# Kernel optimization log

Hardware: AMD Instinct MI355X
Metric: run time of the kernel (lower is better)

Reference implementation:

```python
import jax, jax.numpy as jnp
import numpy as np

N_NODES = 50000
N_EDGES = 800000


def _sage_layer(h, src, dst, ew, Ws, Wn, b, activate):
    # DGL SAGEConv, aggregator_type='mean', with edge weights:
    # message m_e = ew_e * h_src ; neigh = mean over incoming edges (divide by in-degree)
    msg = h[src] * ew[:, None]                       # [E, F] irregular gather
    agg = jax.ops.segment_sum(msg, dst, num_segments=N_NODES)
    deg = jax.ops.segment_sum(jnp.ones_like(ew), dst, num_segments=N_NODES)
    h_neigh = agg / jnp.maximum(deg, 1.0)[:, None]   # zero for isolated nodes
    out = h @ Ws + h_neigh @ Wn + b                  # fc_self + fc_neigh + bias
    return jnp.tanh(out) if activate else out


def setup_inputs() -> dict:
    key = jax.random.key(0)
    ks = jax.random.split(key, 12)
    d = 64
    inp = {
        "b_z": jax.random.normal(ks[0], (N_NODES, d), dtype=jnp.float32),
        "edge_src": jax.random.randint(ks[1], (N_EDGES,), 0, N_NODES, dtype=jnp.int32),
        "edge_dst": jax.random.randint(ks[2], (N_EDGES,), 0, N_NODES, dtype=jnp.int32),
        "edge_weight": jax.random.uniform(ks[3], (N_EDGES,), dtype=jnp.float32),
        "Ws0": jax.random.normal(ks[4], (64, 32), dtype=jnp.float32) / np.sqrt(64),
        "Wn0": jax.random.normal(ks[5], (64, 32), dtype=jnp.float32) / np.sqrt(64),
        "b0": jnp.zeros((32,), jnp.float32),
        "Ws1": jax.random.normal(ks[6], (32, 16), dtype=jnp.float32) / np.sqrt(32),
        "Wn1": jax.random.normal(ks[7], (32, 16), dtype=jnp.float32) / np.sqrt(32),
        "b1": jnp.zeros((16,), jnp.float32),
        "Ws2": jax.random.normal(ks[8], (16, 1), dtype=jnp.float32) / np.sqrt(16),
        "Wn2": jax.random.normal(ks[9], (16, 1), dtype=jnp.float32) / np.sqrt(16),
        "b2": jnp.zeros((1,), jnp.float32),
        "b_size": 500,
    }
    return inp


def reference(b_z, edge_src, edge_dst, edge_weight,
              Ws0, Wn0, b0, Ws1, Wn1, b1, Ws2, Wn2, b2, b_size):
    h = _sage_layer(b_z, edge_src, edge_dst, edge_weight, Ws0, Wn0, b0, True)
    h = _sage_layer(h, edge_src, edge_dst, edge_weight, Ws1, Wn1, b1, True)
    h = _sage_layer(h, edge_src, edge_dst, edge_weight, Ws2, Wn2, b2, False)
    x_hat = h.reshape(b_size, -1)
    return x_hat
```

## Files before the change

### kernel.cpp

```cpp
#include <hip/hip_runtime.h>
#include <hip/hip_bf16.h>

#define N_NODES 50000
#define N_EDGES 800000
#define BLK 256
#define NRANGE 256
#define RNG 196
#define NPART 256
#define EPB 3125
#define PCAP 44
#define SCAP 48

#define EW_SCALE (1.0f / 65535.0f)

__device__ inline void unpack8(uint4 g, float* f) {
    f[0] = __uint_as_float(g.x << 16); f[1] = __uint_as_float(g.x & 0xffff0000u);
    f[2] = __uint_as_float(g.y << 16); f[3] = __uint_as_float(g.y & 0xffff0000u);
    f[4] = __uint_as_float(g.z << 16); f[5] = __uint_as_float(g.z & 0xffff0000u);
    f[6] = __uint_as_float(g.w << 16); f[7] = __uint_as_float(g.w & 0xffff0000u);
}
__device__ inline void unpack4(uint2 g, float* f) {
    f[0] = __uint_as_float(g.x << 16); f[1] = __uint_as_float(g.x & 0xffff0000u);
    f[2] = __uint_as_float(g.y << 16); f[3] = __uint_as_float(g.y & 0xffff0000u);
}

__global__ void pack_premul0_kernel(const int* __restrict__ src,
                                    const float* __restrict__ ew,
                                    unsigned int* __restrict__ pay,
                                    const float* __restrict__ b_z,
                                    const float* __restrict__ Wn0,
                                    const float* __restrict__ Ws0,
                                    const float* __restrict__ b0,
                                    __hip_bfloat16* __restrict__ hW0,
                                    float* __restrict__ hSelf0, int N, int E) {
    int tid = threadIdx.x;
    for (int e = blockIdx.x * BLK + tid; e < E; e += gridDim.x * BLK) {
        unsigned int q = __float2uint_rn(ew[e] * 65535.0f);
        pay[e] = (q << 16) | (unsigned int)src[e];
    }

    __shared__ float sWn[64 * 32];
    __shared__ float sWs[64 * 32];
    __shared__ float sb[32];
    __shared__ float sh[8 * 65];
    for (int i = tid; i < 64 * 32; i += BLK) { sWn[i] = Wn0[i]; sWs[i] = Ws0[i]; }
    if (tid < 32) sb[tid] = b0[tid];
    const int nch = (N + 7) / 8;
    int r = tid >> 5, j = tid & 31;
    for (int c = blockIdx.x; c < nch; c += gridDim.x) {
        __syncthreads();
        int nodeBase = c * 8;
        for (int i = tid; i < 8 * 64; i += BLK) {
            int rr = i >> 6, k = i & 63;
            int n = nodeBase + rr;
            sh[rr * 65 + k] = (n < N) ? b_z[(size_t)n * 64 + k] : 0.f;
        }
        __syncthreads();
        int n = nodeBase + r;
        if (n < N) {
            float an = 0.f, as = 0.f;
#pragma unroll
            for (int k = 0; k < 64; ++k) {
                float hk = sh[r * 65 + k];
                an += hk * sWn[k * 32 + j];
                as += hk * sWs[k * 32 + j];
            }
            hW0[(size_t)n * 32 + j] = __float2bfloat16(an);
            hSelf0[(size_t)n * 32 + j] = as + sb[j];
        }
    }
}

__global__ void partA_kernel(const int* __restrict__ dst,
                             const unsigned int* __restrict__ pay,
                             uint2* __restrict__ lists,
                             int* __restrict__ pcnt) {
    __shared__ uint2 sSorted[EPB];
    __shared__ int hist[NRANGE];
    __shared__ int pfx[NRANGE];
    __shared__ int cur[NRANGE];
    int tid = threadIdx.x;
    int b = blockIdx.x;
    int base = b * EPB;

    hist[tid] = 0;
    __syncthreads();
    for (int i = tid; i < EPB; i += BLK)
        atomicAdd(&hist[dst[base + i] / RNG], 1);
    __syncthreads();
    {
        int v = hist[tid];
        pfx[tid] = v;
        __syncthreads();
        for (int off = 1; off < NRANGE; off <<= 1) {
            int t = (tid >= off) ? pfx[tid - off] : 0;
            __syncthreads();
            pfx[tid] += t;
            __syncthreads();
        }
        int incl = pfx[tid];
        __syncthreads();
        pfx[tid] = incl - v;
        cur[tid] = incl - v;
        __syncthreads();
    }
    for (int i = tid; i < EPB; i += BLK) {
        int e = base + i;
        int d = dst[e];
        int pos = atomicAdd(&cur[d / RNG], 1);
        sSorted[pos] = make_uint2(pay[e], (unsigned int)d);
    }
    __syncthreads();
    for (int i = tid; i < EPB; i += BLK) {
        int lo = 0, hi = NRANGE - 1;
        while (lo < hi) { int mid = (lo + hi + 1) >> 1; if (pfx[mid] <= i) lo = mid; else hi = mid - 1; }
        int idx = i - pfx[lo];
        if (idx < PCAP)
            lists[((size_t)lo * NPART + b) * PCAP + idx] = sSorted[i];
    }
    pcnt[tid * NPART + b] = min(hist[tid], PCAP);
}

__global__ void partB_kernel(const uint2* __restrict__ lists,
                             const int* __restrict__ pcnt,
                             unsigned int* __restrict__ bucket,
                             int* __restrict__ counts, int N) {
    __shared__ unsigned int lslot[RNG * SCAP];
    __shared__ int lcnt[RNG];
    __shared__ int scnt[NPART];
    __shared__ int spfx[NPART];
    int tid = threadIdx.x;
    int r = blockIdx.x;
    int node0 = r * RNG;
    int nn = min(RNG, N - node0);
    if (nn <= 0) return;

    for (int i = tid; i < RNG; i += BLK) lcnt[i] = 0;
    scnt[tid] = pcnt[r * NPART + tid];
    __syncthreads();
    {
        int v = scnt[tid];
        spfx[tid] = v;
        __syncthreads();
        for (int off = 1; off < NPART; off <<= 1) {
            int t = (tid >= off) ? spfx[tid - off] : 0;
            __syncthreads();
            spfx[tid] += t;
            __syncthreads();
        }
        int incl = spfx[tid];
        __syncthreads();
        spfx[tid] = incl - v;
        __syncthreads();
    }
    int T = spfx[NPART - 1] + scnt[NPART - 1];
    for (int j = tid; j < T; j += BLK) {
        int lo = 0, hi = NPART - 1;
        while (lo < hi) { int mid = (lo + hi + 1) >> 1; if (spfx[mid] <= j) lo = mid; else hi = mid - 1; }
        int idx = j - spfx[lo];
        uint2 en = lists[((size_t)r * NPART + lo) * PCAP + idx];
        int node = (int)en.y - node0;
        int pos = atomicAdd(&lcnt[node], 1);
        if (pos < SCAP) lslot[node * SCAP + pos] = en.x;
    }
    __syncthreads();
    unsigned int* __restrict__ gb = bucket + (size_t)node0 * SCAP;
    int tot = nn * SCAP;
    for (int i = tid; i < tot; i += BLK) gb[i] = lslot[i];
    for (int i = tid; i < nn; i += BLK) counts[node0 + i] = min(lcnt[i], SCAP);
}

__global__ void agg0_kernel(const __hip_bfloat16* __restrict__ hW0,
                            const float* __restrict__ hSelf0,
                            const int* __restrict__ cnts,
                            const unsigned int* __restrict__ bucket,
                            const float* __restrict__ Wn1,
                            const float* __restrict__ Ws1,
                            const float* __restrict__ b1,
                            __hip_bfloat16* __restrict__ hW1,
                            float* __restrict__ hSelf1, int N) {
    __shared__ float sWn[32 * 16];
    __shared__ float sWs[32 * 16];
    __shared__ float sb[16];
    __shared__ float sh2[64 * 33];
    int tid = threadIdx.x;
    for (int i = tid; i < 32 * 16; i += BLK) { sWn[i] = Wn1[i]; sWs[i] = Ws1[i]; }
    if (tid < 16) sb[tid] = b1[tid];

    const uint4* __restrict__ tab = (const uint4*)hW0;
    int nodeBase = blockIdx.x * 64;
    int r = tid >> 2;
    int l = tid & 3;
    int n = nodeBase + r;
    if (n < N) {
        int cnt = cnts[n];
        int cn  = min(cnt, SCAP);
        const unsigned int* __restrict__ ep = bucket + (size_t)n * SCAP;
        float acc[8];
#pragma unroll
        for (int t = 0; t < 8; ++t) acc[t] = 0.f;
        int k = 0;
        for (; k + 8 <= cn; k += 8) {
            uint4 ev0 = *(const uint4*)(ep + k);
            uint4 ev1 = *(const uint4*)(ep + k + 4);
            unsigned int ee[8] = { ev0.x, ev0.y, ev0.z, ev0.w,
                                   ev1.x, ev1.y, ev1.z, ev1.w };
            uint4 g[8];
            float w[8];
#pragma unroll
            for (int u = 0; u < 8; ++u) {
                g[u] = tab[(size_t)(ee[u] & 0xffffu) * 4 + l];
                w[u] = (float)(ee[u] >> 16) * EW_SCALE;
            }
#pragma unroll
            for (int u = 0; u < 8; ++u) {
                float f[8];
                unpack8(g[u], f);
#pragma unroll
                for (int t = 0; t < 8; ++t) acc[t] += w[u] * f[t];
            }
        }
        for (; k < cn; ++k) {
            unsigned int e = ep[k];
            float w = (float)(e >> 16) * EW_SCALE;
            uint4 g = tab[(size_t)(e & 0xffffu) * 4 + l];
            float f[8];
            unpack8(g, f);
#pragma unroll
            for (int t = 0; t < 8; ++t) acc[t] += w * f[t];
        }
        float invdeg = 1.0f / fmaxf((float)cnt, 1.0f);
        const float4* __restrict__ hs = (const float4*)(hSelf0 + (size_t)n * 32);
        float4 s0 = hs[l * 2], s1 = hs[l * 2 + 1];
        float sf[8] = { s0.x, s0.y, s0.z, s0.w, s1.x, s1.y, s1.z, s1.w };
#pragma unroll
        for (int t = 0; t < 8; ++t)
            sh2[r * 33 + l * 8 + t] = tanhf(acc[t] * invdeg + sf[t]);
    }
    __syncthreads();
    for (int idx = tid; idx < 64 * 16; idx += BLK) {
        int r2 = idx >> 4, j2 = idx & 15;
        int n2 = nodeBase + r2;
        if (n2 < N) {
            float an = 0.f, as = 0.f;
#pragma unroll
            for (int k = 0; k < 32; ++k) {
                float hk = sh2[r2 * 33 + k];
                an += hk * sWn[k * 16 + j2];
                as += hk * sWs[k * 16 + j2];
            }
            hW1[(size_t)n2 * 16 + j2] = __float2bfloat16(an);
            hSelf1[(size_t)n2 * 16 + j2] = as + sb[j2];
        }
    }
}

__global__ void agg1_kernel(const __hip_bfloat16* __restrict__ hW1,
                            const float* __restrict__ hSelf1,
                            const int* __restrict__ cnts,
                            const unsigned int* __restrict__ bucket,
                            const float* __restrict__ Wn2,
                            const float* __restrict__ Ws2,
                            const float* __restrict__ b2,
                            float* __restrict__ hWf,
                            float* __restrict__ hSelf2, int N) {
    int tid = threadIdx.x;
    int r = tid >> 2;
    int l = tid & 3;
    int n = blockIdx.x * 64 + r;
    if (n >= N) return;

    const uint2* __restrict__ tab = (const uint2*)hW1;
    int cnt = cnts[n];
    int cn  = min(cnt, SCAP);
    const unsigned int* __restrict__ ep = bucket + (size_t)n * SCAP;
    float acc[4];
#pragma unroll
    for (int t = 0; t < 4; ++t) acc[t] = 0.f;
    int k = 0;
    for (; k + 8 <= cn; k += 8) {
        uint4 ev0 = *(const uint4*)(ep + k);
        uint4 ev1 = *(const uint4*)(ep + k + 4);
        unsigned int ee[8] = { ev0.x, ev0.y, ev0.z, ev0.w,
                               ev1.x, ev1.y, ev1.z, ev1.w };
        uint2 g[8];
        float w[8];
#pragma unroll
        for (int u = 0; u < 8; ++u) {
            g[u] = tab[(size_t)(ee[u] & 0xffffu) * 4 + l];
            w[u] = (float)(ee[u] >> 16) * EW_SCALE;
        }
#pragma unroll
        for (int u = 0; u < 8; ++u) {
            float f[4];
            unpack4(g[u], f);
#pragma unroll
            for (int t = 0; t < 4; ++t) acc[t] += w[u] * f[t];
        }
    }
    for (; k < cn; ++k) {
        unsigned int e = ep[k];
        float w = (float)(e >> 16) * EW_SCALE;
        uint2 g = tab[(size_t)(e & 0xffffu) * 4 + l];
        float f[4];
        unpack4(g, f);
#pragma unroll
        for (int t = 0; t < 4; ++t) acc[t] += w * f[t];
    }
    float invdeg = 1.0f / fmaxf((float)cnt, 1.0f);
    const float4* __restrict__ hs = (const float4*)(hSelf1 + (size_t)n * 16);
    float4 sv = hs[l];
    float sf[4] = { sv.x, sv.y, sv.z, sv.w };
    float t2 = 0.f, t3 = 0.f;
#pragma unroll
    for (int t = 0; t < 4; ++t) {
        float hv = tanhf(acc[t] * invdeg + sf[t]);
        t2 += hv * Wn2[l * 4 + t];
        t3 += hv * Ws2[l * 4 + t];
    }
    t2 += __shfl_xor(t2, 1, 4); t2 += __shfl_xor(t2, 2, 4);
    t3 += __shfl_xor(t3, 1, 4); t3 += __shfl_xor(t3, 2, 4);
    if (l == 0) {
        hWf[n] = t2;
        hSelf2[n] = t3 + b2[0];
    }
}

__global__ void agg_final_kernel(const float* __restrict__ hWf,
                                 const float* __restrict__ hSelf2,
                                 const int* __restrict__ cnts,
                                 const unsigned int* __restrict__ bucket,
                                 float* __restrict__ out, int N) {
    int sub = threadIdx.x & 15;
    int r   = threadIdx.x >> 4;
    int n   = blockIdx.x * 16 + r;
    if (n >= N) return;
    int cnt = cnts[n];
    int cn  = min(cnt, SCAP);
    const unsigned int* __restrict__ ep = bucket + (size_t)n * SCAP;
    float a = 0.f;
    for (int k = sub; k < cn; k += 16) {
        unsigned int e = ep[k];
        a += ((float)(e >> 16) * EW_SCALE) * hWf[e & 0xffffu];
    }
#pragma unroll
    for (int m = 8; m >= 1; m >>= 1) a += __shfl_xor(a, m, 16);
    if (sub == 0) {
        float invdeg = 1.0f / fmaxf((float)cnt, 1.0f);
        out[n] = a * invdeg + hSelf2[n];
    }
}

extern "C" void kernel_launch(void* const* d_in, const int* in_sizes, int n_in,
                              void* d_out, int out_size, void* d_ws, size_t ws_size,
                              hipStream_t stream) {
    const float* b_z = (const float*)d_in[0];
    const int*   src = (const int*)d_in[1];
    const int*   dst = (const int*)d_in[2];
    const float* ew  = (const float*)d_in[3];
    const float* Ws0 = (const float*)d_in[4];
    const float* Wn0 = (const float*)d_in[5];
    const float* b0  = (const float*)d_in[6];
    const float* Ws1 = (const float*)d_in[7];
    const float* Wn1 = (const float*)d_in[8];
    const float* b1  = (const float*)d_in[9];
    const float* Ws2 = (const float*)d_in[10];
    const float* Wn2 = (const float*)d_in[11];
    const float* b2  = (const float*)d_in[12];

    const int N = N_NODES;
    const int E = N_EDGES;
    const int GRID_E = 2048;

    unsigned int* pay    = (unsigned int*)d_ws;
    uint2*        lists  = (uint2*)(pay + E);
    int*          pcnt   = (int*)(lists + (size_t)NRANGE * NPART * PCAP);
    int*          counts = pcnt + NRANGE * NPART;
    unsigned int* bucket = (unsigned int*)(counts + N);
    __hip_bfloat16* hW0  = (__hip_bfloat16*)(bucket + (size_t)N * SCAP);
    __hip_bfloat16* hW1  = hW0 + (size_t)N * 32;
    float* hWf    = (float*)(hW1 + (size_t)N * 16);
    float* hSelf0 = hWf + N;
    float* hSelf1 = hSelf0 + (size_t)N * 32;
    float* hSelf2 = hSelf1 + (size_t)N * 16;
    float* outp   = (float*)d_out;

    pack_premul0_kernel<<<GRID_E, BLK, 0, stream>>>(
        src, ew, pay, b_z, Wn0, Ws0, b0, hW0, hSelf0, N, E);
    partA_kernel<<<NPART, BLK, 0, stream>>>(dst, pay, lists, pcnt);
    partB_kernel<<<NRANGE, BLK, 0, stream>>>(lists, pcnt, bucket, counts, N);
    agg0_kernel<<<(N + 63) / 64, BLK, 0, stream>>>(
        hW0, hSelf0, counts, bucket, Wn1, Ws1, b1, hW1, hSelf1, N);
    agg1_kernel<<<(N + 63) / 64, BLK, 0, stream>>>(
        hW1, hSelf1, counts, bucket, Wn2, Ws2, b2, hWf, hSelf2, N);
    agg_final_kernel<<<(N + 15) / 16, BLK, 0, stream>>>(
        hWf, hSelf2, counts, bucket, outp, N);
}
```

Baseline: 105.9 us.

## Fuse layer-0 premultiply with edge partitioning into one block-specialized kernel

Merges the premultiply and payload-pack kernel with the partA edge-partition kernel. The first 256 blocks partition edges and build the packed payload inline from src/ew, while the remaining blocks do the layer-0 dense premultiply. This removes one launch and the global round trip of the intermediate payload array, and lets the two independent jobs overlap. In exchange, the unioned shared-memory buffer is sized for the larger partition branch, which may lower occupancy for the matmul blocks, and the premultiply now runs on fewer blocks.

```diff
diff --git a/kernel.cpp b/kernel.cpp
--- a/kernel.cpp
+++ b/kernel.cpp
@@ -10,6 +10,7 @@
 #define EPB 3125
 #define PCAP 44
 #define SCAP 48
+#define GRID_F 2048
 
 #define EW_SCALE (1.0f / 65535.0f)
 
@@ -24,101 +25,98 @@
     f[2] = __uint_as_float(g.y << 16); f[3] = __uint_as_float(g.y & 0xffff0000u);
 }
 
-__global__ void pack_premul0_kernel(const int* __restrict__ src,
-                                    const float* __restrict__ ew,
-                                    unsigned int* __restrict__ pay,
-                                    const float* __restrict__ b_z,
-                                    const float* __restrict__ Wn0,
-                                    const float* __restrict__ Ws0,
-                                    const float* __restrict__ b0,
-                                    __hip_bfloat16* __restrict__ hW0,
-                                    float* __restrict__ hSelf0, int N, int E) {
+__global__ void premul0_partA_kernel(const float* __restrict__ b_z,
+                                     const int* __restrict__ src,
+                                     const int* __restrict__ dst,
+                                     const float* __restrict__ ew,
+                                     const float* __restrict__ Wn0,
+                                     const float* __restrict__ Ws0,
+                                     const float* __restrict__ b0,
+                                     __hip_bfloat16* __restrict__ hW0,
+                                     float* __restrict__ hSelf0,
+                                     uint2* __restrict__ lists,
+                                     int* __restrict__ pcnt, int N) {
+    __shared__ __align__(16) unsigned char SMEM[28080];
     int tid = threadIdx.x;
-    for (int e = blockIdx.x * BLK + tid; e < E; e += gridDim.x * BLK) {
-        unsigned int q = __float2uint_rn(ew[e] * 65535.0f);
-        pay[e] = (q << 16) | (unsigned int)src[e];
-    }
-
-    __shared__ float sWn[64 * 32];
-    __shared__ float sWs[64 * 32];
-    __shared__ float sb[32];
-    __shared__ float sh[8 * 65];
-    for (int i = tid; i < 64 * 32; i += BLK) { sWn[i] = Wn0[i]; sWs[i] = Ws0[i]; }
-    if (tid < 32) sb[tid] = b0[tid];
-    const int nch = (N + 7) / 8;
-    int r = tid >> 5, j = tid & 31;
-    for (int c = blockIdx.x; c < nch; c += gridDim.x) {
-        __syncthreads();
-        int nodeBase = c * 8;
-        for (int i = tid; i < 8 * 64; i += BLK) {
-            int rr = i >> 6, k = i & 63;
-            int n = nodeBase + rr;
-            sh[rr * 65 + k] = (n < N) ? b_z[(size_t)n * 64 + k] : 0.f;
-        }
-        __syncthreads();
-        int n = nodeBase + r;
-        if (n < N) {
-            float an = 0.f, as = 0.f;
-#pragma unroll
-            for (int k = 0; k < 64; ++k) {
-                float hk = sh[r * 65 + k];
-                an += hk * sWn[k * 32 + j];
-                as += hk * sWs[k * 32 + j];
-            }
-            hW0[(size_t)n * 32 + j] = __float2bfloat16(an);
-            hSelf0[(size_t)n * 32 + j] = as + sb[j];
-        }
-    }
-}
-
-__global__ void partA_kernel(const int* __restrict__ dst,
-                             const unsigned int* __restrict__ pay,
-                             uint2* __restrict__ lists,
-                             int* __restrict__ pcnt) {
-    __shared__ uint2 sSorted[EPB];
-    __shared__ int hist[NRANGE];
-    __shared__ int pfx[NRANGE];
-    __shared__ int cur[NRANGE];
-    int tid = threadIdx.x;
-    int b = blockIdx.x;
-    int base = b * EPB;
-
-    hist[tid] = 0;
-    __syncthreads();
-    for (int i = tid; i < EPB; i += BLK)
-        atomicAdd(&hist[dst[base + i] / RNG], 1);
-    __syncthreads();
-    {
-        int v = hist[tid];
-        pfx[tid] = v;
-        __syncthreads();
-        for (int off = 1; off < NRANGE; off <<= 1) {
-            int t = (tid >= off) ? pfx[tid - off] : 0;
-            __syncthreads();
-            pfx[tid] += t;
-            __syncthreads();
-        }
-        int incl = pfx[tid];
-        __syncthreads();
-        pfx[tid] = incl - v;
-        cur[tid] = incl - v;
-        __syncthreads();
-    }
-    for (int i = tid; i < EPB; i += BLK) {
-        int e = base + i;
-        int d = dst[e];
-        int pos = atomicAdd(&cur[d / RNG], 1);
-        sSorted[pos] = make_uint2(pay[e], (unsigned int)d);
-    }
-    __syncthreads();
-    for (int i = tid; i < EPB; i += BLK) {
-        int lo = 0, hi = NRANGE - 1;
-        while (lo < hi) { int mid = (lo + hi + 1) >> 1; if (pfx[mid] <= i) lo = mid; else hi = mid - 1; }
-        int idx = i - pfx[lo];
-        if (idx < PCAP)
-            lists[((size_t)lo * NPART + b) * PCAP + idx] = sSorted[i];
-    }
-    pcnt[tid * NPART + b] = min(hist[tid], PCAP);
+    int bid = blockIdx.x;
+
+    if (bid < NPART) {
+        uint2* sSorted = (uint2*)SMEM;
+        int* hist = (int*)(SMEM + 25000);
+        int* pfx  = (int*)(SMEM + 26024);
+        int* cur  = (int*)(SMEM + 27048);
+        int base = bid * EPB;
+        hist[tid] = 0;
+        __syncthreads();
+        for (int i = tid; i < EPB; i += BLK)
+            atomicAdd(&hist[dst[base + i] / RNG], 1);
+        __syncthreads();
+        {
+            int v = hist[tid];
+            pfx[tid] = v;
+            __syncthreads();
+            for (int off = 1; off < NRANGE; off <<= 1) {
+                int t = (tid >= off) ? pfx[tid - off] : 0;
+                __syncthreads();
+                pfx[tid] += t;
+                __syncthreads();
+            }
+            int incl = pfx[tid];
+            __syncthreads();
+            pfx[tid] = incl - v;
+            cur[tid] = incl - v;
+            __syncthreads();
+        }
+        for (int i = tid; i < EPB; i += BLK) {
+            int e = base + i;
+            int d = dst[e];
+            unsigned int q = __float2uint_rn(ew[e] * 65535.0f);
+            unsigned int py = (q << 16) | (unsigned int)src[e];
+            int pos = atomicAdd(&cur[d / RNG], 1);
+            sSorted[pos] = make_uint2(py, (unsigned int)d);
+        }
+        __syncthreads();
+        for (int i = tid; i < EPB; i += BLK) {
+            int lo = 0, hi = NRANGE - 1;
+            while (lo < hi) { int mid = (lo + hi + 1) >> 1; if (pfx[mid] <= i) lo = mid; else hi = mid - 1; }
+            int idx = i - pfx[lo];
+            if (idx < PCAP)
+                lists[((size_t)lo * NPART + bid) * PCAP + idx] = sSorted[i];
+        }
+        pcnt[tid * NPART + bid] = min(hist[tid], PCAP);
+    } else {
+        float* sWn = (float*)SMEM;
+        float* sWs = (float*)(SMEM + 8192);
+        float* sb  = (float*)(SMEM + 16384);
+        float* sh  = (float*)(SMEM + 16512);
+        for (int i = tid; i < 64 * 32; i += BLK) { sWn[i] = Wn0[i]; sWs[i] = Ws0[i]; }
+        if (tid < 32) sb[tid] = b0[tid];
+        const int nch = (N + 7) / 8;
+        const int stride = GRID_F - NPART;
+        int r = tid >> 5, j = tid & 31;
+        for (int c = bid - NPART; c < nch; c += stride) {
+            __syncthreads();
+            int nodeBase = c * 8;
+            for (int i = tid; i < 8 * 64; i += BLK) {
+                int rr = i >> 6, k = i & 63;
+                int n = nodeBase + rr;
+                sh[rr * 65 + k] = (n < N) ? b_z[(size_t)n * 64 + k] : 0.f;
+            }
+            __syncthreads();
+            int n = nodeBase + r;
+            if (n < N) {
+                float an = 0.f, as = 0.f;
+#pragma unroll
+                for (int k = 0; k < 64; ++k) {
+                    float hk = sh[r * 65 + k];
+                    an += hk * sWn[k * 32 + j];
+                    as += hk * sWs[k * 32 + j];
+                }
+                hW0[(size_t)n * 32 + j] = __float2bfloat16(an);
+                hSelf0[(size_t)n * 32 + j] = as + sb[j];
+            }
+        }
+    }
 }
 
 __global__ void partB_kernel(const uint2* __restrict__ lists,
@@ -369,11 +367,8 @@
     const float* b2  = (const float*)d_in[12];
 
     const int N = N_NODES;
-    const int E = N_EDGES;
-    const int GRID_E = 2048;
-
-    unsigned int* pay    = (unsigned int*)d_ws;
-    uint2*        lists  = (uint2*)(pay + E);
+
+    uint2*        lists  = (uint2*)d_ws;
     int*          pcnt   = (int*)(lists + (size_t)NRANGE * NPART * PCAP);
     int*          counts = pcnt + NRANGE * NPART;
     unsigned int* bucket = (unsigned int*)(counts + N);
@@ -385,9 +380,8 @@
     float* hSelf2 = hSelf1 + (size_t)N * 16;
     float* outp   = (float*)d_out;
 
-    pack_premul0_kernel<<<GRID_E, BLK, 0, stream>>>(
-        src, ew, pay, b_z, Wn0, Ws0, b0, hW0, hSelf0, N, E);
-    partA_kernel<<<NPART, BLK, 0, stream>>>(dst, pay, lists, pcnt);
+    premul0_partA_kernel<<<GRID_F, BLK, 0, stream>>>(
+        b_z, src, dst, ew, Wn0, Ws0, b0, hW0, hSelf0, lists, pcnt, N);
     partB_kernel<<<NRANGE, BLK, 0, stream>>>(lists, pcnt, bucket, counts, N);
     agg0_kernel<<<(N + 63) / 64, BLK, 0, stream>>>(
         hW0, hSelf0, counts, bucket, Wn1, Ws1, b1, hW1, hSelf1, N);
```

After: 89.32 us (median of 2 runs). 15.6% less time.
